# Performance work log

Measured on AMD Instinct MI355X. Metric: run time of the kernel, lower is better.

The kernel has to match this reference:

```python
import jax, jax.numpy as jnp
import numpy as np

EPS = 1e-12  # torch F.normalize eps


def setup_inputs() -> dict:
    key = jax.random.key(0)
    k1, k2, k3, k4, k5 = jax.random.split(key, 5)
    N, C, H, W = 32, 512, 32, 32
    E = 1024   # expansion * dim
    G = 8      # group
    D = E // G # 128, per-group channel dim
    K = 64     # num_clusters
    x = jax.random.normal(k1, (N, C, H, W), dtype=jnp.float32)
    W1 = jax.random.normal(k2, (E, C), dtype=jnp.float32) / np.sqrt(C)
    W2 = jax.random.normal(k3, (G, E), dtype=jnp.float32) / np.sqrt(E)
    Wc = jax.random.normal(k4, (K, D), dtype=jnp.float32) / np.sqrt(D)
    centroids = jax.random.uniform(k5, (K, D), dtype=jnp.float32)
    return {"x": x, "W1": W1, "W2": W2, "Wc": Wc, "centroids": centroids}


def reference(x, W1, W2, Wc, centroids):
    # x: [N, C, H, W]; W1: [E, C]; W2: [G, E]; Wc: [K, D]; centroids: [K, D]
    N, C, H, W = x.shape
    E = W1.shape[0]
    G = W2.shape[0]
    K, D = Wc.shape
    P = H * W
    # descriptor-wise L2 normalization over channel dim
    norm = jnp.linalg.norm(x, axis=1, keepdims=True)
    x = x / jnp.maximum(norm, EPS)
    # linear1 on channels: [N, E, P]
    xe = jnp.einsum('ncp,ec->nep', x.reshape(N, C, P), W1)
    # grouped features: [N, G, D, P]
    xg = xe.reshape(N, G, D, P)
    # attention gate: sigmoid(linear2)  -> [N, G, P]
    att = jax.nn.sigmoid(jnp.einsum('nep,ge->ngp', xe, W2))
    # 1x1 conv = per-pixel matmul with cluster weights -> [N, G, K, P]
    soft_assign = jax.nn.softmax(jnp.einsum('ngdp,kd->ngkp', xg, Wc), axis=2)
    # combined per-(cluster,pixel) weight
    w = soft_assign * att[:, :, None, :]  # [N, G, K, P]
    # NetVLAD residual aggregation, algebraically decomposed to avoid the
    # giant [N,G,K,D,P] intermediate:
    #   vlad[n,k,d] = sum_{g,p} w * xg  -  centroids[k,d] * sum_{g,p} w
    agg = jnp.einsum('ngkp,ngdp->nkd', w, xg)  # [N, K, D]
    wsum = w.sum(axis=(1, 3))                  # [N, K]
    vlad = agg - wsum[:, :, None] * centroids[None]  # [N, K, D]
    return vlad.reshape(N, K * D)
```

## Files before the change

### kernel.cpp

```cpp
#include <hip/hip_runtime.h>


#define N_  32
#define C_  512
#define P_  1024
#define E_  1024
#define G_  8
#define D_  128
#define K_  64

typedef __attribute__((ext_vector_type(8))) short bf16x8;
typedef __attribute__((ext_vector_type(4))) float f32x4;

__device__ __forceinline__ unsigned short f2b(float f) {
    union { float f; unsigned u; } v; v.f = f;
    unsigned r = (v.u + 0x7FFFu + ((v.u >> 16) & 1u)) >> 16;
    return (unsigned short)r;
}
__device__ __forceinline__ float b2f(unsigned short h) {
    union { unsigned u; float f; } v; v.u = ((unsigned)h) << 16;
    return v.f;
}

__device__ __forceinline__ void gl_lds16(const void* g, void* l) {
    __builtin_amdgcn_global_load_lds(
        (const __attribute__((address_space(1))) void*)g,
        (__attribute__((address_space(3))) void*)l, 16, 0, 0);
}

__global__ __launch_bounds__(256) void k0_prep(const float* __restrict__ W1,
                                               const float* __restrict__ Wc,
                                               unsigned short* __restrict__ W1b,
                                               unsigned short* __restrict__ Vb) {
    int bid = blockIdx.x;
    int t = threadIdx.x;
    int i0 = bid * 512 + t;
    W1b[i0]       = f2b(W1[i0]);
    W1b[i0 + 256] = f2b(W1[i0 + 256]);
    int ch = bid & 1, k = (bid >> 1) & 63, g = bid >> 7;
    int c = ch * 256 + t;
    float acc = 0.f;
    #pragma unroll 8
    for (int d = 0; d < 128; ++d)
        acc += Wc[k * 128 + d] * W1[(g * 128 + d) * C_ + c];
    Vb[(g * 64 + k) * C_ + c] = f2b(acc);
}

__global__ __launch_bounds__(256) void k1_norm_transpose(const float* __restrict__ x,
                                                         unsigned short* __restrict__ xhat_t) {
    __shared__ short xc[128 * 256];
    __shared__ float red[256];
    __shared__ float rn[64];
    int n = blockIdx.y;
    int p0 = blockIdx.x * 64;
    int t = threadIdx.x;
    int ps = t & 63, cs = t >> 6;

    float ss = 0.f;
    for (int i = 0; i < 128; ++i) {
        float v = x[((size_t)(n * C_ + cs * 128 + i)) * P_ + p0 + ps];
        ss += v * v;
        xc[i * 256 + t] = (short)f2b(v);
    }
    red[t] = ss;
    __syncthreads();
    if (t < 64) {
        float s = red[t] + red[64 + t] + red[128 + t] + red[192 + t];
        rn[t] = 1.0f / fmaxf(sqrtf(s), 1e-12f);
    }
    __syncthreads();

    float r = rn[ps];
    size_t base = ((size_t)(n * P_ + p0 + ps)) * C_ + cs * 128;
    #pragma unroll
    for (int jj = 0; jj < 16; ++jj) {
        bf16x8 o;
        #pragma unroll
        for (int j = 0; j < 8; ++j)
            o[j] = (short)f2b(b2f((unsigned short)xc[(jj * 8 + j) * 256 + t]) * r);
        *(bf16x8*)&xhat_t[base + jj * 8] = o;
    }
}

__global__ __launch_bounds__(256) void k2_gemm_xe(const unsigned short* __restrict__ W1b,
                                                  const unsigned short* __restrict__ xhat_t,
                                                  unsigned short* __restrict__ xe) {
    __shared__ __align__(16) short As[128 * 64];
    __shared__ __align__(16) short Bs[128 * 64];
    int n = blockIdx.y;
    int e0 = (blockIdx.x >> 3) * 128;
    int p0 = (blockIdx.x & 7) * 128;
    int t = threadIdx.x;
    int w = t >> 6, l = t & 63, q = l >> 4, l15 = l & 15;
    int wr = w >> 1, wc = w & 1;

    f32x4 acc[4][4];
    #pragma unroll
    for (int mi = 0; mi < 4; ++mi)
        #pragma unroll
        for (int ni = 0; ni < 4; ++ni)
            acc[mi][ni] = (f32x4){0.f, 0.f, 0.f, 0.f};

    for (int ks = 0; ks < 8; ++ks) {
        int k0 = ks * 64;
        #pragma unroll
        for (int i = 0; i < 4; ++i) {
            int ch = i * 256 + t;
            int row = ch >> 3, c8 = ch & 7;
            gl_lds16(&W1b[(e0 + row) * C_ + k0 + ((c8 ^ (row & 7)) * 8)], &As[ch * 8]);
        }
        #pragma unroll
        for (int i = 0; i < 4; ++i) {
            int ch = i * 256 + t;
            int row = ch >> 3, c8 = ch & 7;
            gl_lds16(&xhat_t[((size_t)(n * P_ + p0 + row)) * C_ + k0 + ((c8 ^ (row & 7)) * 8)], &Bs[ch * 8]);
        }
        __syncthreads();

        #pragma unroll
        for (int kk = 0; kk < 2; ++kk) {
            bf16x8 af[4], bf[4];
            #pragma unroll
            for (int mi = 0; mi < 4; ++mi)
                af[mi] = *(const bf16x8*)&As[(wr * 64 + mi * 16 + l15) * 64 + (((kk * 4 + q) ^ (l15 & 7)) * 8)];
            #pragma unroll
            for (int ni = 0; ni < 4; ++ni)
                bf[ni] = *(const bf16x8*)&Bs[(wc * 64 + ni * 16 + l15) * 64 + (((kk * 4 + q) ^ (l15 & 7)) * 8)];
            #pragma unroll
            for (int mi = 0; mi < 4; ++mi)
                #pragma unroll
                for (int ni = 0; ni < 4; ++ni)
                    acc[mi][ni] = __builtin_amdgcn_mfma_f32_16x16x32_bf16(af[mi], bf[ni], acc[mi][ni], 0, 0, 0);
        }
        __syncthreads();
    }

    #pragma unroll
    for (int mi = 0; mi < 4; ++mi) {
        #pragma unroll
        for (int ni = 0; ni < 4; ++ni) {
            #pragma unroll
            for (int r = 0; r < 4; ++r) {
                int e = e0 + wr * 64 + mi * 16 + q * 4 + r;
                int p = p0 + wc * 64 + ni * 16 + l15;
                xe[((size_t)(n * E_ + e)) * P_ + p] = f2b(acc[mi][ni][r]);
            }
        }
    }
}

__global__ __launch_bounds__(256) void k3a_att_part(const unsigned short* __restrict__ xe,
                                                    const float* __restrict__ W2,
                                                    float* __restrict__ att_part) {
    int n = blockIdx.y;
    int ec = blockIdx.x;
    int t = threadIdx.x;
    int e0 = ec * 64;
    f32x4 acc[8];
    #pragma unroll
    for (int g = 0; g < 8; ++g) acc[g] = (f32x4){0.f, 0.f, 0.f, 0.f};
    #pragma unroll 4
    for (int i = 0; i < 64; ++i) {
        int e = e0 + i;
        ushort4 v4 = *(const ushort4*)&xe[((size_t)(n * E_ + e)) * P_ + t * 4];
        f32x4 vf = {b2f(v4.x), b2f(v4.y), b2f(v4.z), b2f(v4.w)};
        #pragma unroll
        for (int g = 0; g < 8; ++g)
            acc[g] += vf * W2[g * E_ + e];
    }
    #pragma unroll
    for (int g = 0; g < 8; ++g)
        *(f32x4*)&att_part[(((size_t)(n * 16 + ec)) * 8 + g) * P_ + t * 4] = acc[g];
}

__global__ __launch_bounds__(256) void k3b_att_reduce(const float* __restrict__ att_part,
                                                      float* __restrict__ att_s) {
    int idx = blockIdx.x * 256 + threadIdx.x;
    int p = idx & 1023;
    int g = (idx >> 10) & 7;
    int n = idx >> 13;
    float s = 0.f;
    #pragma unroll
    for (int ec = 0; ec < 16; ++ec)
        s += att_part[(((size_t)(n * 16 + ec)) * 8 + g) * P_ + p];
    att_s[idx] = 1.0f / (1.0f + __expf(-s));
}

__global__ __launch_bounds__(512, 4) void k4_assign_agg(const unsigned short* __restrict__ Vb,
                                                        const unsigned short* __restrict__ xhat_t,
                                                        const unsigned short* __restrict__ xe,
                                                        const float* __restrict__ att_s,
                                                        float* __restrict__ agg_part,
                                                        float* __restrict__ wsum_part) {
    __shared__ __align__(16) char smem[8192 + 16384 + 32768];
    short* As2   = (short*)smem;
    short* Bs2   = (short*)(smem + 8192);
    short* xglds = (short*)(smem + 24576);
    short* wlds  = (short*)smem;
    float* wred  = (float*)smem;

    int b = blockIdx.y * 16 + blockIdx.x;
    int work = (b & 7) * 64 + (b >> 3);
    int n = work >> 4, g = work & 7, ph = (work >> 3) & 1;

    int t = threadIdx.x;
    int w = t >> 6, l = t & 63, q = l >> 4, l15 = l & 15;
    int kh = w >> 2, dq = w & 3;

    f32x4 acc_a[2][2];
    #pragma unroll
    for (int mi = 0; mi < 2; ++mi)
        #pragma unroll
        for (int ni = 0; ni < 2; ++ni)
            acc_a[mi][ni] = (f32x4){0.f, 0.f, 0.f, 0.f};
    float wsp[16];
    #pragma unroll
    for (int j = 0; j < 16; ++j) wsp[j] = 0.f;

    for (int cc = 0; cc < 4; ++cc) {
        int p0c = ph * 512 + cc * 128;

        #pragma unroll
        for (int i = 0; i < 4; ++i) {
            int ch = i * 512 + t;
            int row = ch >> 4, c16 = ch & 15;
            gl_lds16(&xe[((size_t)(n * E_ + g * 128 + row)) * P_ + p0c + ((c16 ^ (row & 7)) * 8)],
                     &xglds[ch * 8]);
        }

        f32x4 acc_s[4];
        #pragma unroll
        for (int mi = 0; mi < 4; ++mi)
            acc_s[mi] = (f32x4){0.f, 0.f, 0.f, 0.f};

        for (int ks = 0; ks < 8; ++ks) {
            int k0 = ks * 64;
            {
                int row = t >> 3, c8 = t & 7;
                gl_lds16(&Vb[(g * 64 + row) * C_ + k0 + ((c8 ^ (row & 7)) * 8)], &As2[t * 8]);
            }
            #pragma unroll
            for (int i = 0; i < 2; ++i) {
                int ch = i * 512 + t;
                int row = ch >> 3, c8 = ch & 7;
                gl_lds16(&xhat_t[((size_t)(n * P_ + p0c + row)) * C_ + k0 + ((c8 ^ (row & 7)) * 8)], &Bs2[ch * 8]);
            }
            __syncthreads();
            #pragma unroll
            for (int kk = 0; kk < 2; ++kk) {
                bf16x8 af[4], bfr;
                #pragma unroll
                for (int mi = 0; mi < 4; ++mi)
                    af[mi] = *(const bf16x8*)&As2[(mi * 16 + l15) * 64 + (((kk * 4 + q) ^ (l15 & 7)) * 8)];
                bfr = *(const bf16x8*)&Bs2[(w * 16 + l15) * 64 + (((kk * 4 + q) ^ (l15 & 7)) * 8)];
                #pragma unroll
                for (int mi = 0; mi < 4; ++mi)
                    acc_s[mi] = __builtin_amdgcn_mfma_f32_16x16x32_bf16(af[mi], bfr, acc_s[mi], 0, 0, 0);
            }
            __syncthreads();
        }

        {
            float m = -1e30f;
            #pragma unroll
            for (int mi = 0; mi < 4; ++mi)
                #pragma unroll
                for (int r = 0; r < 4; ++r)
                    m = fmaxf(m, acc_s[mi][r]);
            m = fmaxf(m, __shfl_xor(m, 16));
            m = fmaxf(m, __shfl_xor(m, 32));
            float s = 0.f;
            #pragma unroll
            for (int mi = 0; mi < 4; ++mi)
                #pragma unroll
                for (int r = 0; r < 4; ++r) {
                    float e = __expf(acc_s[mi][r] - m);
                    acc_s[mi][r] = e;
                    s += e;
                }
            s += __shfl_xor(s, 16);
            s += __shfl_xor(s, 32);

            float av = att_s[(((size_t)(n * G_ + g)) * P_) + p0c + w * 16 + l15];
            float scale = av / s;

            #pragma unroll
            for (int mi = 0; mi < 4; ++mi)
                #pragma unroll
                for (int r = 0; r < 4; ++r) {
                    float wv = acc_s[mi][r] * scale;
                    wsp[mi * 4 + r] += wv;
                    wlds[(mi * 16 + q * 4 + r) * 136 + (w * 16 + l15)] = (short)f2b(wv);
                }
        }
        __syncthreads();

        #pragma unroll
        for (int pk = 0; pk < 4; ++pk) {
            bf16x8 a2[2], b2[2];
            #pragma unroll
            for (int mi = 0; mi < 2; ++mi)
                a2[mi] = *(const bf16x8*)&wlds[(kh * 32 + mi * 16 + l15) * 136 + pk * 32 + q * 8];
            #pragma unroll
            for (int ni = 0; ni < 2; ++ni)
                b2[ni] = *(const bf16x8*)&xglds[(dq * 32 + ni * 16 + l15) * 128
                                                + (((pk * 4 + q) ^ (l15 & 7)) * 8)];
            #pragma unroll
            for (int mi = 0; mi < 2; ++mi)
                #pragma unroll
                for (int ni = 0; ni < 2; ++ni)
                    acc_a[mi][ni] = __builtin_amdgcn_mfma_f32_16x16x32_bf16(a2[mi], b2[ni], acc_a[mi][ni], 0, 0, 0);
        }
        __syncthreads();
    }

    size_t base = (((size_t)(n * G_ + g)) * 2 + ph) * 64;
    #pragma unroll
    for (int mi = 0; mi < 2; ++mi)
        #pragma unroll
        for (int ni = 0; ni < 2; ++ni)
            #pragma unroll
            for (int r = 0; r < 4; ++r) {
                int k = kh * 32 + mi * 16 + q * 4 + r;
                int d = dq * 32 + ni * 16 + l15;
                agg_part[(base + k) * 128 + d] = acc_a[mi][ni][r];
            }

    #pragma unroll
    for (int j = 0; j < 16; ++j) {
        float v = wsp[j];
        v += __shfl_xor(v, 1);
        v += __shfl_xor(v, 2);
        v += __shfl_xor(v, 4);
        v += __shfl_xor(v, 8);
        if (l15 == 0) {
            int k = (j >> 2) * 16 + q * 4 + (j & 3);
            wred[w * 64 + k] = v;
        }
    }
    __syncthreads();
    if (t < 64) {
        float s = 0.f;
        #pragma unroll
        for (int wv = 0; wv < 8; ++wv)
            s += wred[wv * 64 + t];
        wsum_part[(((size_t)(n * G_ + g)) * 2 + ph) * 64 + t] = s;
    }
}

__global__ __launch_bounds__(256) void k5_final(const float* __restrict__ agg_part,
                                                const float* __restrict__ wsum_part,
                                                const float* __restrict__ centroids,
                                                float* __restrict__ out) {
    int idx = blockIdx.x * 256 + threadIdx.x;
    int d = idx & 127;
    int k = (idx >> 7) & 63;
    int n = idx >> 13;
    float ws = 0.f;
    #pragma unroll
    for (int g = 0; g < 8; ++g)
        #pragma unroll
        for (int ph = 0; ph < 2; ++ph)
            ws += wsum_part[(((size_t)(n * G_ + g)) * 2 + ph) * 64 + k];
    float agg = 0.f;
    #pragma unroll
    for (int g = 0; g < 8; ++g)
        #pragma unroll
        for (int ph = 0; ph < 2; ++ph)
            agg += agg_part[(((((size_t)(n * G_ + g)) * 2 + ph) * 64) + k) * 128 + d];
    out[idx] = agg - ws * centroids[k * 128 + d];
}

extern "C" void kernel_launch(void* const* d_in, const int* in_sizes, int n_in,
                              void* d_out, int out_size, void* d_ws, size_t ws_size,
                              hipStream_t stream) {
    const float* x         = (const float*)d_in[0];
    const float* W1        = (const float*)d_in[1];
    const float* W2        = (const float*)d_in[2];
    const float* Wc        = (const float*)d_in[3];
    const float* centroids = (const float*)d_in[4];
    float* out = (float*)d_out;

    char* ws = (char*)d_ws;
    unsigned short* W1b      = (unsigned short*)(ws + 0);
    unsigned short* Vb       = (unsigned short*)(ws + 1048576);
    unsigned short* xhat_t   = (unsigned short*)(ws + 1572864);
    unsigned short* xe       = (unsigned short*)(ws + 35127296);
    float*          att_s    = (float*)(ws + 102236160);
    float*          att_part = (float*)(ws + 103284736);
    float*          agg_part = (float*)(ws + 103284736);
    float*          wsum_part= (float*)(ws + 120061952);

    hipLaunchKernelGGL(k0_prep,        dim3(1024), dim3(256), 0, stream, W1, Wc, W1b, Vb);
    hipLaunchKernelGGL(k1_norm_transpose, dim3(16, 32), dim3(256), 0, stream, x, xhat_t);
    hipLaunchKernelGGL(k2_gemm_xe,     dim3(64, 32), dim3(256), 0, stream, W1b, xhat_t, xe);
    hipLaunchKernelGGL(k3a_att_part,   dim3(16, 32), dim3(256), 0, stream, xe, W2, att_part);
    hipLaunchKernelGGL(k3b_att_reduce, dim3(1024), dim3(256), 0, stream, att_part, att_s);
    hipLaunchKernelGGL(k4_assign_agg,  dim3(16, 32), dim3(512), 0, stream, Vb, xhat_t, xe,
                       att_s, agg_part, wsum_part);
    hipLaunchKernelGGL(k5_final,       dim3(1024), dim3(256), 0, stream,
                       agg_part, wsum_part, centroids, out);
}
```

Measured before the change: 233.3 us.

## Double-buffer LDS staging in assign-agg kernel with explicit vmcnt waits

```diff
diff --git a/kernel.cpp b/kernel.cpp
--- a/kernel.cpp
+++ b/kernel.cpp
@@ -27,6 +27,9 @@
         (const __attribute__((address_space(1))) void*)g,
         (__attribute__((address_space(3))) void*)l, 16, 0, 0);
 }
+
+#define SB  __builtin_amdgcn_sched_barrier(0)
+#define BAR __builtin_amdgcn_s_barrier()
 
 __global__ __launch_bounds__(256) void k0_prep(const float* __restrict__ W1,
                                                const float* __restrict__ Wc,
@@ -186,16 +189,57 @@
     att_s[idx] = 1.0f / (1.0f + __expf(-s));
 }
 
+__device__ __forceinline__ void stage_s(short* sb, const unsigned short* __restrict__ Vb,
+                                        const unsigned short* __restrict__ xhat_t,
+                                        int g, int n, int p0c, int k0, int t) {
+    {
+        int row = t >> 3, c8 = t & 7;
+        gl_lds16(&Vb[(g * 64 + row) * C_ + k0 + ((c8 ^ (row & 7)) * 8)], &sb[t * 8]);
+    }
+    #pragma unroll
+    for (int i = 0; i < 2; ++i) {
+        int ch = i * 512 + t;
+        int row = ch >> 3, c8 = ch & 7;
+        gl_lds16(&xhat_t[((size_t)(n * P_ + p0c + row)) * C_ + k0 + ((c8 ^ (row & 7)) * 8)],
+                 &sb[4096 + ch * 8]);
+    }
+}
+
+__device__ __forceinline__ void stage_xg(short* xglds, const unsigned short* __restrict__ xe,
+                                         int n, int g, int p0c, int t) {
+    #pragma unroll
+    for (int i = 0; i < 4; ++i) {
+        int ch = i * 512 + t;
+        int row = ch >> 4, c16 = ch & 15;
+        gl_lds16(&xe[((size_t)(n * E_ + g * 128 + row)) * P_ + p0c + ((c16 ^ (row & 7)) * 8)],
+                 &xglds[ch * 8]);
+    }
+}
+
+__device__ __forceinline__ void mfma_s(f32x4 acc[4], const short* sb, int w, int q, int l15) {
+    #pragma unroll
+    for (int kk = 0; kk < 2; ++kk) {
+        bf16x8 af[4], bfr;
+        #pragma unroll
+        for (int mi = 0; mi < 4; ++mi)
+            af[mi] = *(const bf16x8*)&sb[(mi * 16 + l15) * 64 + (((kk * 4 + q) ^ (l15 & 7)) * 8)];
+        bfr = *(const bf16x8*)&sb[4096 + (w * 16 + l15) * 64 + (((kk * 4 + q) ^ (l15 & 7)) * 8)];
+        #pragma unroll
+        for (int mi = 0; mi < 4; ++mi)
+            acc[mi] = __builtin_amdgcn_mfma_f32_16x16x32_bf16(af[mi], bfr, acc[mi], 0, 0, 0);
+    }
+}
+
 __global__ __launch_bounds__(512, 4) void k4_assign_agg(const unsigned short* __restrict__ Vb,
                                                         const unsigned short* __restrict__ xhat_t,
                                                         const unsigned short* __restrict__ xe,
                                                         const float* __restrict__ att_s,
                                                         float* __restrict__ agg_part,
                                                         float* __restrict__ wsum_part) {
-    __shared__ __align__(16) char smem[8192 + 16384 + 32768];
-    short* As2   = (short*)smem;
-    short* Bs2   = (short*)(smem + 8192);
-    short* xglds = (short*)(smem + 24576);
+    __shared__ __align__(16) char smem[81920];
+    short* S0    = (short*)smem;
+    short* S1    = (short*)(smem + 24576);
+    short* xglds = (short*)(smem + 49152);
     short* wlds  = (short*)smem;
     float* wred  = (float*)smem;
 
@@ -217,48 +261,39 @@
     #pragma unroll
     for (int j = 0; j < 16; ++j) wsp[j] = 0.f;
 
+#define WAITV(n_) asm volatile("s_waitcnt vmcnt(" #n_ ")" ::: "memory")
+#define RND(CUR, NXT, KN) \
+    stage_s(NXT, Vb, xhat_t, g, n, p0c, (KN) * 64, t); \
+    WAITV(3); BAR; SB; \
+    mfma_s(acc_s, CUR, w, q, l15); \
+    BAR; SB;
+
+    #pragma unroll 1
     for (int cc = 0; cc < 4; ++cc) {
         int p0c = ph * 512 + cc * 128;
 
-        #pragma unroll
-        for (int i = 0; i < 4; ++i) {
-            int ch = i * 512 + t;
-            int row = ch >> 4, c16 = ch & 15;
-            gl_lds16(&xe[((size_t)(n * E_ + g * 128 + row)) * P_ + p0c + ((c16 ^ (row & 7)) * 8)],
-                     &xglds[ch * 8]);
-        }
+        float av = att_s[(((size_t)(n * G_ + g)) * P_) + p0c + w * 16 + l15];
 
         f32x4 acc_s[4];
         #pragma unroll
         for (int mi = 0; mi < 4; ++mi)
             acc_s[mi] = (f32x4){0.f, 0.f, 0.f, 0.f};
 
-        for (int ks = 0; ks < 8; ++ks) {
-            int k0 = ks * 64;
-            {
-                int row = t >> 3, c8 = t & 7;
-                gl_lds16(&Vb[(g * 64 + row) * C_ + k0 + ((c8 ^ (row & 7)) * 8)], &As2[t * 8]);
-            }
-            #pragma unroll
-            for (int i = 0; i < 2; ++i) {
-                int ch = i * 512 + t;
-                int row = ch >> 3, c8 = ch & 7;
-                gl_lds16(&xhat_t[((size_t)(n * P_ + p0c + row)) * C_ + k0 + ((c8 ^ (row & 7)) * 8)], &Bs2[ch * 8]);
-            }
-            __syncthreads();
-            #pragma unroll
-            for (int kk = 0; kk < 2; ++kk) {
-                bf16x8 af[4], bfr;
-                #pragma unroll
-                for (int mi = 0; mi < 4; ++mi)
-                    af[mi] = *(const bf16x8*)&As2[(mi * 16 + l15) * 64 + (((kk * 4 + q) ^ (l15 & 7)) * 8)];
-                bfr = *(const bf16x8*)&Bs2[(w * 16 + l15) * 64 + (((kk * 4 + q) ^ (l15 & 7)) * 8)];
-                #pragma unroll
-                for (int mi = 0; mi < 4; ++mi)
-                    acc_s[mi] = __builtin_amdgcn_mfma_f32_16x16x32_bf16(af[mi], bfr, acc_s[mi], 0, 0, 0);
-            }
-            __syncthreads();
-        }
+        stage_s(S0, Vb, xhat_t, g, n, p0c, 0, t);
+        RND(S0, S1, 1)
+        RND(S1, S0, 2)
+        RND(S0, S1, 3)
+        RND(S1, S0, 4)
+        RND(S0, S1, 5)
+        RND(S1, S0, 6)
+        stage_s(S1, Vb, xhat_t, g, n, p0c, 448, t);
+        stage_xg(xglds, xe, n, g, p0c, t);
+        WAITV(7); BAR; SB;
+        mfma_s(acc_s, S0, w, q, l15);
+        BAR; SB;
+        WAITV(4); BAR; SB;
+        mfma_s(acc_s, S1, w, q, l15);
+        BAR; SB;
 
         {
             float m = -1e30f;
@@ -281,7 +316,6 @@
             s += __shfl_xor(s, 16);
             s += __shfl_xor(s, 32);
 
-            float av = att_s[(((size_t)(n * G_ + g)) * P_) + p0c + w * 16 + l15];
             float scale = av / s;
 
             #pragma unroll
```

Result: no change. 230.7 us (-1.1%).
